# Kernel optimization log

Measured on AMD Instinct MI355X. Metric: run time of the kernel, lower is better.

Reference implementation:

```python
import jax, jax.numpy as jnp
import numpy as np

IN_FEATURES = 4096
OUT_FEATURES = 12288
INT8_MAX = 127.0


def setup_inputs() -> dict:
    key = jax.random.key(0)
    kx, kw, ks, kb = jax.random.split(key, 4)
    x = jax.random.normal(kx, (8192, IN_FEATURES), dtype=jnp.float32)
    # pre-quantized int8 weight, stored [out_features, in_features] like the torch module
    weight = jax.random.randint(kw, (OUT_FEATURES, IN_FEATURES), -127, 128, dtype=jnp.int8)
    # per-output-channel weight scale, [out_features, 1]
    weight_scale = (jax.random.uniform(ks, (OUT_FEATURES, 1), dtype=jnp.float32) * 0.02 + 1e-4)
    bias = jax.random.normal(kb, (OUT_FEATURES,), dtype=jnp.float32) * 0.01
    return {"x": x, "weight": weight, "weight_scale": weight_scale, "bias": bias}


def _dynamic_int8_quant(x):
    # symmetric per-token quantization: scale = amax(|x|) / 127
    amax = jnp.max(jnp.abs(x), axis=-1, keepdims=True)  # [M, 1]
    scale = jnp.maximum(amax, 1e-8) / INT8_MAX
    x_q = jnp.clip(jnp.round(x / scale), -INT8_MAX, INT8_MAX).astype(jnp.int8)
    return x_q, scale


def reference(x, weight, weight_scale, bias):
    x_q, x_scale = _dynamic_int8_quant(x)                    # [M,K] int8, [M,1] f32
    # int8 GEMM with int32 accumulation: [M,K] @ [K,N]
    acc = jnp.matmul(x_q.astype(jnp.int32), weight.T.astype(jnp.int32))  # [M,N] int32
    # epilogue: dequant with per-token and per-channel scales, then bias add
    out = acc.astype(jnp.float32) * x_scale * weight_scale[:, 0][None, :] + bias[None, :]
    return out.astype(x.dtype)
```

## Files before the change

### kernel.cpp

```cpp
#include <hip/hip_runtime.h>
#include <stdint.h>

#define M_DIM 8192
#define K_DIM 4096
#define N_DIM 12288

typedef int v4i __attribute__((ext_vector_type(4)));

#define GLDS16(g, l)                                                         \
  __builtin_amdgcn_global_load_lds(                                          \
      (const __attribute__((address_space(1))) void*)(g),                    \
      (__attribute__((address_space(3))) void*)(l), 16, 0, 0)

#define BARRIER() asm volatile("s_barrier" ::: "memory")
#define VMCNT2() asm volatile("s_waitcnt vmcnt(2)" ::: "memory")
#define VMCNT0() asm volatile("s_waitcnt vmcnt(0)" ::: "memory")

__global__ __launch_bounds__(256) void prep(const float* __restrict__ x,
                                            int8_t* __restrict__ xq,
                                            float* __restrict__ xs,
                                            const int* __restrict__ w32,
                                            int8_t* __restrict__ w8) {
  const int t = threadIdx.x;
  if ((int)blockIdx.x < M_DIM) {
    const int row = blockIdx.x;
    const float* xr = x + (size_t)row * K_DIM;

    float4 v[4];
    float amax = 0.f;
#pragma unroll
    for (int i = 0; i < 4; ++i) {
      v[i] = reinterpret_cast<const float4*>(xr)[t * 4 + i];
      amax = fmaxf(amax, fmaxf(fmaxf(fabsf(v[i].x), fabsf(v[i].y)),
                               fmaxf(fabsf(v[i].z), fabsf(v[i].w))));
    }
#pragma unroll
    for (int off = 32; off > 0; off >>= 1)
      amax = fmaxf(amax, __shfl_xor(amax, off));

    __shared__ float smax[4];
    if ((t & 63) == 0) smax[t >> 6] = amax;
    __syncthreads();
    amax = fmaxf(fmaxf(smax[0], smax[1]), fmaxf(smax[2], smax[3]));

    const float scale = fmaxf(amax, 1e-8f) / 127.f;

    union {
      int8_t b[16];
      v4i v;
    } p;
    const float* pv = reinterpret_cast<const float*>(v);
#pragma unroll
    for (int i = 0; i < 16; ++i) {
      float r = rintf(pv[i] / scale);
      r = fminf(127.f, fmaxf(-127.f, r));
      p.b[i] = (int8_t)(int)r;
    }
    reinterpret_cast<v4i*>(xq + (size_t)row * K_DIM)[t] = p.v;
    if (t == 0) xs[row] = scale;
  } else {
    const size_t i = (((size_t)blockIdx.x - M_DIM) * 256 + t) * 16;
    const int4* src = reinterpret_cast<const int4*>(w32 + i);
    union {
      int8_t b[16];
      v4i v;
    } p;
#pragma unroll
    for (int c = 0; c < 4; ++c) {
      int4 q = src[c];
      p.b[c * 4 + 0] = (int8_t)q.x;
      p.b[c * 4 + 1] = (int8_t)q.y;
      p.b[c * 4 + 2] = (int8_t)q.z;
      p.b[c * 4 + 3] = (int8_t)q.w;
    }
    *reinterpret_cast<v4i*>(w8 + i) = p.v;
  }
}

#define BM 256
#define BN 256
#define BKB 128
#define NTILES (K_DIM / BKB)

__global__ __launch_bounds__(512, 2) void gemm_i8(
    const int8_t* __restrict__ xq, const float* __restrict__ xs,
    const int8_t* __restrict__ w8, const float* __restrict__ wsc,
    const float* __restrict__ bias, float* __restrict__ out) {
  __shared__ __align__(16) int8_t lds[131072];
  const v4i* Lv = (const v4i*)lds;

  const int t = threadIdx.x;
  const int lane = t & 63;
  const int w = t >> 6;
  const int wr = w >> 2;
  const int wc = w & 3;
  const int fr = lane & 15;
  const int kq = lane >> 4;
  const int l7 = lane & 7;

  const int NT_N = N_DIM / BN;
  const int nwg = (M_DIM / BM) * NT_N;
  int bid = (int)blockIdx.x;
  bid = (bid & 7) * (nwg >> 3) + (bid >> 3);
  const int rowBase = (bid / NT_N) * BM;
  const int colBase = (bid % NT_N) * BN;

  const int srow = t >> 3;
  const int gslot = (t & 7) ^ (srow & 7);
  const int8_t* gA = xq + (size_t)(rowBase + srow) * K_DIM + gslot * 16;
  const int8_t* gB = w8 + (size_t)(colBase + srow) * K_DIM + gslot * 16;
  int8_t* ldsw = lds + w * 1024;

#define STAGE_A(c, r0, k0) \
  GLDS16(gA + (size_t)(r0) * K_DIM + (k0), ldsw + (c) * 32768 + (r0) * 128)
#define STAGE_B(c, r0, k0) \
  GLDS16(gB + (size_t)(r0) * K_DIM + (k0), ldsw + 65536 + (c) * 32768 + (r0) * 128)

  const int s0_ = kq ^ l7;
  const int s1_ = s0_ ^ 4;
  const int rA = wr * 128 + fr;
  const int rB = wc * 64 + fr;

#define LA(c, mh, mi, ks) \
  Lv[((c) << 11) + ((rA + (mh) * 64 + (mi) * 16) << 3) + ((ks) ? s1_ : s0_)]
#define LB(c, ni, ks) \
  Lv[4096 + ((c) << 11) + ((rB + (ni) * 16) << 3) + ((ks) ? s1_ : s0_)]

  v4i acc[8][4];
#pragma unroll
  for (int i = 0; i < 8; ++i)
#pragma unroll
    for (int j = 0; j < 4; ++j) acc[i][j] = (v4i){0, 0, 0, 0};

  STAGE_B(0, 0, 0); STAGE_B(0, 64, 0); STAGE_B(0, 128, 0); STAGE_B(0, 192, 0);
  STAGE_A(0, 0, 0); STAGE_A(0, 128, 0); STAGE_A(0, 64, 0); STAGE_A(0, 192, 0);
  VMCNT2();
  BARRIER();

  v4i af[4], bf[4];

#define PHASE(c, MH, KS, LOADB, STG, WAIT)                                    \
  {                                                                           \
    _Pragma("unroll") for (int mi = 0; mi < 4; ++mi)                          \
        af[mi] = LA(c, MH, mi, KS);                                           \
    if (LOADB) {                                                              \
      _Pragma("unroll") for (int ni = 0; ni < 4; ++ni)                        \
          bf[ni] = LB(c, ni, KS);                                             \
    }                                                                         \
    STG;                                                                      \
    BARRIER();                                                                \
    __builtin_amdgcn_s_setprio(1);                                            \
    _Pragma("unroll") for (int ni = 0; ni < 4; ++ni)                          \
        _Pragma("unroll") for (int mi = 0; mi < 4; ++mi)                      \
            acc[(MH) * 4 + mi][ni] = __builtin_amdgcn_mfma_i32_16x16x64_i8(   \
                af[mi], bf[ni], acc[(MH) * 4 + mi][ni], 0, 0, 0);             \
    __builtin_amdgcn_s_setprio(0);                                            \
    WAIT;                                                                     \
    BARRIER();                                                                \
  }

  for (int tt = 0; tt < NTILES - 1; ++tt) {
    const int c = tt & 1;
    const int d = c ^ 1;
    const int k1 = (tt + 1) * BKB;
    PHASE(c, 0, 0, 1, { STAGE_B(d, 0, k1); STAGE_B(d, 64, k1); }, VMCNT2());
    PHASE(c, 1, 0, 0, { STAGE_B(d, 128, k1); STAGE_B(d, 192, k1); }, );
    PHASE(c, 0, 1, 1, { STAGE_A(d, 0, k1); STAGE_A(d, 128, k1); }, );
    PHASE(c, 1, 1, 0, { STAGE_A(d, 64, k1); STAGE_A(d, 192, k1); }, VMCNT2());
  }
  {
    PHASE(1, 0, 0, 1, , VMCNT0());
    PHASE(1, 1, 0, 0, , );
    PHASE(1, 0, 1, 1, , );
    PHASE(1, 1, 1, 0, , );
  }

  const int orow0 = rowBase + wr * 128;
  const int ocol0 = colBase + wc * 64;
  const int rsub = kq * 4;
#pragma unroll
  for (int mi8 = 0; mi8 < 8; ++mi8) {
    const int r0 = orow0 + mi8 * 16 + rsub;
    float s4[4];
#pragma unroll
    for (int r = 0; r < 4; ++r) s4[r] = xs[r0 + r];
#pragma unroll
    for (int ni = 0; ni < 4; ++ni) {
      const int col = ocol0 + ni * 16 + fr;
      const float wf = wsc[col];
      const float bb = bias[col];
#pragma unroll
      for (int r = 0; r < 4; ++r)
        out[(size_t)(r0 + r) * N_DIM + col] =
            (float)acc[mi8][ni][r] * s4[r] * wf + bb;
    }
  }
}

extern "C" void kernel_launch(void* const* d_in, const int* in_sizes, int n_in,
                              void* d_out, int out_size, void* d_ws,
                              size_t ws_size, hipStream_t stream) {
  const float* x = (const float*)d_in[0];
  const int* w32 = (const int*)d_in[1];
  const float* wscale = (const float*)d_in[2];
  const float* bias = (const float*)d_in[3];
  float* out = (float*)d_out;

  int8_t* xq = (int8_t*)d_ws;
  float* xs = (float*)((char*)d_ws + (size_t)M_DIM * K_DIM);
  int8_t* w8 = (int8_t*)((char*)d_ws + (size_t)M_DIM * K_DIM + M_DIM * 4);

  const int packBlocks = (N_DIM * K_DIM) / (256 * 16);
  prep<<<M_DIM + packBlocks, 256, 0, stream>>>(x, xq, xs, w32, w8);
  gemm_i8<<<(M_DIM / BM) * (N_DIM / BN), 512, 0, stream>>>(xq, xs, w8, wscale,
                                                           bias, out);
}
```

Measured before the change: 503.5 us.

## Remap workgroups to XCD-local tile groups and unroll double-buffer loop by two

Replaces the old block-id swizzle with a mapping in which each XCD owns a 4x8 group of output tiles, so workgroups sharing A rows and B columns land on the same L2. It also unrolls the K loop by two so the buffer index is a compile-time constant, and precomputes LDS fragment base pointers so reads use immediate offsets. The goal is better L2 reuse and less address arithmetic in the inner loop, at the cost of larger code. The mapping assumes 32x48 tiles split in a specific way across 8 XCDs.

After: 461.2 us. -8.4%, faster.

```diff
diff --git a/kernel.cpp b/kernel.cpp
--- a/kernel.cpp
+++ b/kernel.cpp
@@ -87,7 +87,6 @@
     const int8_t* __restrict__ w8, const float* __restrict__ wsc,
     const float* __restrict__ bias, float* __restrict__ out) {
   __shared__ __align__(16) int8_t lds[131072];
-  const v4i* Lv = (const v4i*)lds;
 
   const int t = threadIdx.x;
   const int lane = t & 63;
@@ -98,12 +97,15 @@
   const int kq = lane >> 4;
   const int l7 = lane & 7;
 
-  const int NT_N = N_DIM / BN;
-  const int nwg = (M_DIM / BM) * NT_N;
-  int bid = (int)blockIdx.x;
-  bid = (bid & 7) * (nwg >> 3) + (bid >> 3);
-  const int rowBase = (bid / NT_N) * BM;
-  const int colBase = (bid % NT_N) * BN;
+  {
+  }
+  const int bid = (int)blockIdx.x;
+  const int xcd = bid & 7;
+  const int q = bid >> 3;
+  const int g = q >> 5;
+  const int j = q & 31;
+  const int rowBase = (xcd * 4 + (j >> 3)) * BM;
+  const int colBase = (g * 8 + (j & 7)) * BN;
 
   const int srow = t >> 3;
   const int gslot = (t & 7) ^ (srow & 7);
@@ -121,16 +123,16 @@
   const int rA = wr * 128 + fr;
   const int rB = wc * 64 + fr;
 
-#define LA(c, mh, mi, ks) \
-  Lv[((c) << 11) + ((rA + (mh) * 64 + (mi) * 16) << 3) + ((ks) ? s1_ : s0_)]
-#define LB(c, ni, ks) \
-  Lv[4096 + ((c) << 11) + ((rB + (ni) * 16) << 3) + ((ks) ? s1_ : s0_)]
+  const v4i* pA0 = (const v4i*)lds + ((rA << 3) + s0_);
+  const v4i* pA1 = (const v4i*)lds + ((rA << 3) + s1_);
+  const v4i* pB0 = (const v4i*)(lds + 65536) + ((rB << 3) + s0_);
+  const v4i* pB1 = (const v4i*)(lds + 65536) + ((rB << 3) + s1_);
 
   v4i acc[8][4];
 #pragma unroll
   for (int i = 0; i < 8; ++i)
 #pragma unroll
-    for (int j = 0; j < 4; ++j) acc[i][j] = (v4i){0, 0, 0, 0};
+    for (int jj = 0; jj < 4; ++jj) acc[i][jj] = (v4i){0, 0, 0, 0};
 
   STAGE_B(0, 0, 0); STAGE_B(0, 64, 0); STAGE_B(0, 128, 0); STAGE_B(0, 192, 0);
   STAGE_A(0, 0, 0); STAGE_A(0, 128, 0); STAGE_A(0, 64, 0); STAGE_A(0, 192, 0);
@@ -141,11 +143,17 @@
 
 #define PHASE(c, MH, KS, LOADB, STG, WAIT)                                    \
   {                                                                           \
-    _Pragma("unroll") for (int mi = 0; mi < 4; ++mi)                          \
-        af[mi] = LA(c, MH, mi, KS);                                           \
+    const v4i* _pa = (KS) ? pA1 : pA0;                                        \
+    af[0] = _pa[((c) << 11) + (((MH)*64 + 0) << 3)];                          \
+    af[1] = _pa[((c) << 11) + (((MH)*64 + 16) << 3)];                         \
+    af[2] = _pa[((c) << 11) + (((MH)*64 + 32) << 3)];                         \
+    af[3] = _pa[((c) << 11) + (((MH)*64 + 48) << 3)];                         \
     if (LOADB) {                                                              \
-      _Pragma("unroll") for (int ni = 0; ni < 4; ++ni)                        \
-          bf[ni] = LB(c, ni, KS);                                             \
+      const v4i* _pb = (KS) ? pB1 : pB0;                                      \
+      bf[0] = _pb[((c) << 11) + (0 << 3)];                                    \
+      bf[1] = _pb[((c) << 11) + (16 << 3)];                                   \
+      bf[2] = _pb[((c) << 11) + (32 << 3)];                                   \
+      bf[3] = _pb[((c) << 11) + (48 << 3)];                                   \
     }                                                                         \
     STG;                                                                      \
     BARRIER();                                                                \
@@ -159,15 +167,19 @@
     BARRIER();                                                                \
   }
 
-  for (int tt = 0; tt < NTILES - 1; ++tt) {
-    const int c = tt & 1;
-    const int d = c ^ 1;
-    const int k1 = (tt + 1) * BKB;
-    PHASE(c, 0, 0, 1, { STAGE_B(d, 0, k1); STAGE_B(d, 64, k1); }, VMCNT2());
-    PHASE(c, 1, 0, 0, { STAGE_B(d, 128, k1); STAGE_B(d, 192, k1); }, );
-    PHASE(c, 0, 1, 1, { STAGE_A(d, 0, k1); STAGE_A(d, 128, k1); }, );
-    PHASE(c, 1, 1, 0, { STAGE_A(d, 64, k1); STAGE_A(d, 192, k1); }, VMCNT2());
-  }
+#define TILE(c, d, k1)                                                        \
+  PHASE(c, 0, 0, 1, { STAGE_B(d, 0, k1); STAGE_B(d, 64, k1); }, VMCNT2());    \
+  PHASE(c, 1, 0, 0, { STAGE_B(d, 128, k1); STAGE_B(d, 192, k1); }, );         \
+  PHASE(c, 0, 1, 1, { STAGE_A(d, 0, k1); STAGE_A(d, 128, k1); }, );           \
+  PHASE(c, 1, 1, 0, { STAGE_A(d, 64, k1); STAGE_A(d, 192, k1); }, VMCNT2());
+
+  for (int tt = 0; tt < NTILES - 2; tt += 2) {
+    const int k1a = (tt + 1) * BKB;
+    const int k1b = (tt + 2) * BKB;
+    TILE(0, 1, k1a);
+    TILE(1, 0, k1b);
+  }
+  TILE(0, 1, (NTILES - 1) * BKB);
   {
     PHASE(1, 0, 0, 1, , VMCNT0());
     PHASE(1, 1, 0, 0, , );
```
